# Kernel tuning notes

Hardware: AMD Instinct MI355X
Metric: run time of the kernel (lower is better)

Reference implementation:

```python
import jax, jax.numpy as jnp
import numpy as np

SC = 19          # window stride/size (non-kitti)
K = 3 * SC       # 57, unfold kernel size
CH = 128         # chnn

def conv2d(x, w, b=None, pad=(0, 0)):
    y = jax.lax.conv_general_dilated(
        x, w, (1, 1), [(pad[0], pad[0]), (pad[1], pad[1])],
        dimension_numbers=('NCHW', 'OIHW', 'NCHW'))
    return y if b is None else y + b[None, :, None, None]

def unfold(x):
    # nn.Unfold(kernel_size=3*SC, padding=SC, stride=SC) -> [b, c, K*K, h_sc*w_sc]
    b, c, h, w = x.shape
    h_sc, w_sc = h // SC, w // SC
    xp = jnp.pad(x, ((0, 0), (0, 0), (SC, SC), (SC, SC)))
    ii = np.arange(h_sc)[:, None] * SC + np.arange(K)[None, :]
    jj = np.arange(w_sc)[:, None] * SC + np.arange(K)[None, :]
    p = xp[:, :, ii, :][:, :, :, :, jj]              # [b,c,h_sc,K,w_sc,K]
    return p.transpose(0, 1, 3, 5, 2, 4).reshape(b, c, K * K, h_sc * w_sc)

def to_windows(x):
    # [b,c,h,w] -> [b,c,h_sc*w_sc, SC*SC] (non-overlapping SCxSC windows)
    b, c, h, w = x.shape
    h_sc, w_sc = h // SC, w // SC
    return x.reshape(b, c, h_sc, SC, w_sc, SC).transpose(0, 1, 2, 4, 3, 5).reshape(b, c, h_sc * w_sc, SC * SC)

def fs_kernel(w_prelu, b, h, w):
    # geometric falloff kernel, separable in x/y: [b, K*K, L, SC*SC]
    a = w_prelu[0] * 0.02      # scp = 0.02
    half = 2.0 * SC            # half_ker
    crd = jnp.arange(K, dtype=jnp.float32)
    idx_x = SC + jnp.arange(w, dtype=jnp.float32) % SC
    idx_y = SC + jnp.arange(h, dtype=jnp.float32) % SC
    def falloff(d):
        v = d - half
        pre = jnp.where(v > 0, v, a * v)   # PReLU
        return jnp.maximum(1.0 - pre, 0.0) # -prelu + b(=1), clamped at 0
    ox = falloff(jnp.abs(crd[:, None] - idx_x[None, :]))  # [K, w]
    oy = falloff(jnp.abs(crd[:, None] - idx_y[None, :]))  # [K, h]
    ker = oy[:, None, :, None] * ox[None, :, None, :]      # [Ky, Kx, h, w]
    ker = jnp.broadcast_to(ker[None], (b, K, K, h, w)).reshape(b, K * K, h, w)
    return to_windows(ker)

def kpa(feat_ci, feat_mi, w_qk, w_v, gamma, w_prelu):
    b, c, h_in, w_in = feat_mi.shape
    x_pad = SC - w_in % SC
    y_pad = SC - h_in % SC
    pad4 = ((0, 0), (0, 0), (0, y_pad), (0, x_pad))
    feat_c = jnp.pad(feat_ci, pad4)
    feat_m = jnp.pad(feat_mi, pad4)
    h, w = h_in + y_pad, w_in + x_pad
    h_sc, w_sc = h // SC, w // SC
    # validity mask -> additive -99 bias for padded keys/queries
    fm = jnp.pad(jnp.ones((1, 1, h_in, w_in), feat_mi.dtype), pad4)
    fm_k = unfold(fm)                                  # [1,1,K^2,L]
    fm_q = to_windows(fm)                              # [1,1,L,SC^2]
    am = (fm_k[:, 0, :, :, None] * fm_q[:, 0, None, :, :] - 1.0) * 99.0
    # itr == 0 path: compute attention
    qk = conv2d(feat_c, w_qk)
    feat_q, feat_k = qk[:, :c], qk[:, c:]
    feat_k = unfold(feat_k) * (c ** -0.5)              # [b,c,K^2,L]
    feat_q = to_windows(feat_q)                        # [b,c,L,SC^2]
    attn = jnp.einsum('bckn,bcns->bkns', feat_k, feat_q) + am
    attn = jax.nn.softmax(fs_kernel(w_prelu, b, h, w) * attn, axis=1)
    feat_v = unfold(conv2d(feat_m, w_v))               # [b,c,K^2,L]
    feat_r = jnp.einsum('bkns,bckn->bcns', attn, feat_v)  # [b,c,L,SC^2]
    feat_r = feat_r.reshape(b, c, h_sc, w_sc, SC, SC).transpose(0, 1, 2, 4, 3, 5).reshape(b, c, h, w)
    return feat_mi + feat_r[:, :, :h_in, :w_in] * gamma[0]

def sep_conv_gru(h, x, wz1, bz1, wr1, br1, wq1, bq1, wz2, bz2, wr2, br2, wq2, bq2):
    hx = jnp.concatenate([h, x], 1)
    z = jax.nn.sigmoid(conv2d(hx, wz1, bz1, (0, 2)))
    r = jax.nn.sigmoid(conv2d(hx, wr1, br1, (0, 2)))
    q = jnp.tanh(conv2d(jnp.concatenate([r * h, x], 1), wq1, bq1, (0, 2)))
    h = (1 - z) * h + z * q
    hx = jnp.concatenate([h, x], 1)
    z = jax.nn.sigmoid(conv2d(hx, wz2, bz2, (2, 0)))
    r = jax.nn.sigmoid(conv2d(hx, wr2, br2, (2, 0)))
    q = jnp.tanh(conv2d(jnp.concatenate([r * h, x], 1), wq2, bq2, (2, 0)))
    return (1 - z) * h + z * q

PARAM_SHAPES = [
    ('w_cor1', (256, 324, 1, 1)), ('b_cor1', (256,)), ('w_cor2', (192, 256, 3, 3)), ('b_cor2', (192,)),
    ('w_flo1', (128, 2, 7, 7)), ('b_flo1', (128,)), ('w_flo2', (64, 128, 3, 3)), ('b_flo2', (64,)),
    ('w_mo', (126, 256, 3, 3)), ('b_mo', (126,)),
    ('w_qk', (256, 128, 1, 1)), ('w_v', (128, 128, 1, 1)),
    ('wz1', (128, 512, 1, 5)), ('bz1', (128,)), ('wr1', (128, 512, 1, 5)), ('br1', (128,)),
    ('wq1', (128, 512, 1, 5)), ('bq1', (128,)),
    ('wz2', (128, 512, 5, 1)), ('bz2', (128,)), ('wr2', (128, 512, 5, 1)), ('br2', (128,)),
    ('wq2', (128, 512, 5, 1)), ('bq2', (128,)),
    ('w_f1', (256, 128, 3, 3)), ('b_f1', (256,)), ('w_f2', (2, 256, 3, 3)), ('b_f2', (2,)),
    ('w_m1', (256, 128, 3, 3)), ('b_m1', (256,)), ('w_m2', (576, 256, 1, 1)), ('b_m2', (576,)),
]

def setup_inputs() -> dict:
    key = jax.random.key(0)
    B, H, W = 2, 55, 128
    ks = jax.random.split(key, len(PARAM_SHAPES) + 4)
    inp = {
        'net': jax.random.normal(ks[0], (B, CH, H, W), jnp.float32),
        'inp': jax.random.normal(ks[1], (B, CH, H, W), jnp.float32),
        'corr': jax.random.normal(ks[2], (B, 324, H, W), jnp.float32),
        'flow': jax.random.normal(ks[3], (B, 2, H, W), jnp.float32),
    }
    for i, (name, shp) in enumerate(PARAM_SHAPES):
        fan_in = int(np.prod(shp[1:])) if len(shp) > 1 else shp[0]
        scale = 1.0 / np.sqrt(fan_in) if len(shp) > 1 else 0.01
        inp[name] = scale * jax.random.normal(ks[4 + i], shp, jnp.float32)
    inp['gamma'] = jnp.array([0.5], jnp.float32)            # nonzero so KPA contributes
    inp['w_prelu'] = jnp.array([1.0 / 28.0], jnp.float32)    # 1 / h_k, h_k = (3*SC-1)/2
    inp['itr'] = 0
    return inp

def reference(net, inp, corr, flow, w_cor1, b_cor1, w_cor2, b_cor2, w_flo1, b_flo1, w_flo2, b_flo2, w_mo, b_mo, w_qk, w_v, wz1, bz1, wr1, br1, wq1, bq1, wz2, bz2, wr2, br2, wq2, bq2, w_f1, b_f1, w_f2, b_f2, w_m1, b_m1, w_m2, b_m2, gamma, w_prelu, itr):
    # _mo_enc
    fc = jax.nn.relu(conv2d(corr, w_cor1, b_cor1))
    fc = jax.nn.relu(conv2d(fc, w_cor2, b_cor2, (1, 1)))
    ff = jax.nn.relu(conv2d(flow, w_flo1, b_flo1, (3, 3)))
    ff = jax.nn.relu(conv2d(ff, w_flo2, b_flo2, (1, 1)))
    fm = jax.nn.relu(conv2d(jnp.concatenate([fc, ff], 1), w_mo, b_mo, (1, 1)))
    feat_mo = jnp.concatenate([fm, flow], 1)           # [b,128,h,w]
    # KPA attention (itr == 0)
    feat_moa = kpa(inp, feat_mo, w_qk, w_v, gamma, w_prelu)
    x = jnp.concatenate([inp, feat_mo, feat_moa], 1)   # [b,384,h,w]
    net = sep_conv_gru(net, x, wz1, bz1, wr1, br1, wq1, bq1, wz2, bz2, wr2, br2, wq2, bq2)
    d = jax.nn.relu(conv2d(net, w_f1, b_f1, (1, 1)))
    delta_flow = conv2d(d, w_f2, b_f2, (1, 1))
    m = jax.nn.relu(conv2d(net, w_m1, b_m1, (1, 1)))
    mask = 0.25 * conv2d(m, w_m2, b_m2)
    return net, mask, delta_flow
```

## Files before the change

### kernel.cpp

```cpp
#include <hip/hip_runtime.h>
#include <hip/hip_bf16.h>

typedef __bf16 bf16;
typedef __attribute__((ext_vector_type(8))) __bf16 v8bf;
typedef __attribute__((ext_vector_type(4))) float f32x4;
typedef __attribute__((ext_vector_type(16))) float f32x16;

#define HH 55
#define WW 128
#define HWP 7040
#define BHW 14080
#define QS 0.08838834764831845f
#define LOG2E 1.4426950408889634f

__device__ __forceinline__ void g2l16(const bf16* g, bf16* l){
  __builtin_amdgcn_global_load_lds(
      (const __attribute__((address_space(1))) void*)g,
      (__attribute__((address_space(3))) void*)l, 16, 0, 0);
}

#define NCV 17
__device__ const int PK_CinSrc[NCV] = {324,256,128,256,128,128,512,512,512,512,512,512,128,128,256,256,98};
__device__ const int PK_Kc[NCV]     = {384,256,128,256,128,128,512,512,512,512,512,512,128,128,256,256,128};
__device__ const int PK_ntap[NCV]   = {1,9,9,9,1,1,5,5,5,5,5,5,9,9,9,1,1};
__device__ const int PK_Ctot[NCV]   = {256,256,128,128,256,128,256,256,128,256,256,128,512,512,128,640,128};
__device__ const int PK_coB[NCV]    = {0,0,0,0,0,0,0,128,0,0,128,0,0,256,0,0,0};
__device__ const int PK_dst[NCV]    = {0,98304,688128,835584,1130496,1163264,1179648,1179648,
  1835008,2162688,2162688,2818048,3145728,3145728,3735552,4030464,4194304};
__device__ const int PKD_cum[NCV+1] = {0,98304,540672,614400,904704,937472,953856,
  1281536,1609216,1936896,2264576,2592256,2919936,3214848,3509760,3514368,3661824,3678208};
__device__ const int PKD_Co[NCV]    = {256,192,64,126,256,128,128,128,128,128,128,128,256,256,2,576,128};

__device__ const int PB_off[15]={0,256,512,640,1152,1280,1408,1536,1664,1792,1920,2176,2432,2560,3200};
__device__ const int PB_cnt[15]={256,192,64,126,128,128,128,128,128,128,256,256,2,576,128};

struct W17 { const float* w[17]; };
struct B15 { const float* b[15]; };

struct XP {
  W17 wp; B15 bp;
  const float *net, *inp, *corr, *flow;
  bf16 *Bp; float *bias;
  bf16 *hx; float *hcur; bf16 *corr_cl; bf16 *im2c;
};

__global__ __launch_bounds__(256) void init_k(XP X){
  __shared__ float T[64][65];
  int bid = blockIdx.x;
  const int t = threadIdx.x;
  if (bid < 14368){
    int idx = bid*256 + t;
    int c = 0;
    while (idx >= PKD_cum[c+1]) ++c;
    int local = idx - PKD_cum[c];
    if (c == 16){
      int co = local >> 7, k = local & 127;
      if (k < 98)
        X.Bp[PK_dst[16] + co*128 + k] = (bf16)X.wp.w[16][co*98 + (k&1)*49 + (k>>1)];
      return;
    }
    int Kc = PK_Kc[c];
    int CKc = PKD_Co[c]*Kc;
    int tap = local / CKc;
    int rem = local - tap*CKc;
    int co = rem / Kc;
    int ci = rem - co*Kc;
    int cs = PK_CinSrc[c];
    if (ci < cs){
      float v = X.wp.w[c][(co*cs + ci)*PK_ntap[c] + tap];
      if (c == 4 && co < 128) v *= QS;
      X.Bp[PK_dst[c] + (tap*PK_Ctot[c] + PK_coB[c] + co)*Kc + ci] = (bf16)v;
    }
    return;
  }
  bid -= 14368;
  if (bid < 880){
    int pt = bid%110, ct = (bid/110)&3, b = bid/440;
    const float* src = (ct < 2) ? X.net : X.inp;
    int c0s = (ct & 1)*64;
    int cbase = (ct < 2) ? 0 : 128;
    int p0 = pt*64;
    int pj = t & 63, cr4 = t >> 6;
#pragma unroll
    for (int i=0;i<16;++i)
      T[cr4 + i*4][pj] = src[((size_t)b*128 + c0s + cr4 + i*4)*HWP + p0 + pj];
    __syncthreads();
    int cj = t & 63, pr4 = t >> 6;
#pragma unroll
    for (int i=0;i<16;++i){
      int pp = p0 + pr4 + i*4;
      float v = T[cj][pr4 + i*4];
      X.hx[((size_t)(b*HWP+pp))*512 + cbase + c0s + cj] = (bf16)v;
      if (ct < 2) X.hcur[((size_t)(b*HWP+pp))*128 + c0s + cj] = v;
    }
    return;
  }
  bid -= 880;
  if (bid < 1320){
    int pt = bid%110, ct = (bid/110)%6, b = bid/660;
    int p0 = pt*64, c0s = ct*64;
    int pj = t & 63, cr4 = t >> 6;
#pragma unroll
    for (int i=0;i<16;++i){
      int c = c0s + cr4 + i*4;
      float v = 0.f;
      if (c < 324) v = X.corr[((size_t)b*324 + c)*HWP + p0 + pj];
      T[cr4 + i*4][pj] = v;
    }
    __syncthreads();
    int cj = t & 63, pr4 = t >> 6;
#pragma unroll
    for (int i=0;i<16;++i){
      int pp = p0 + pr4 + i*4;
      int cc = c0s + cj;
      X.corr_cl[((size_t)(b*HWP+pp))*384 + cc] = (bf16)T[cj][pr4 + i*4];
    }
    return;
  }
  bid -= 1320;
  if (bid < 110){
    int i = bid*256 + t;
    int c = i & 1, p = i >> 1;
    int b = p / HWP, pix = p - b*HWP;
    X.hx[(size_t)p*512 + 382 + c] = (bf16)X.flow[(b*2+c)*HWP + pix];
    return;
  }
  bid -= 110;
  if (bid < 7040){
    int i = bid*256 + t;
    int k = i & 127, p = i >> 7;
    int b = p / HWP, pix = p - b*HWP, y = pix >> 7, x = pix & 127;
    float v = 0.f;
    if (k < 98){
      int tap = k >> 1, c2 = k & 1, kh = tap/7, kw = tap - 7*(tap/7);
      int yy = y + kh - 3, xx = x + kw - 3;
      if ((unsigned)yy < 55u && (unsigned)xx < 128u) v = X.flow[(b*2+c2)*HWP + yy*128 + xx];
    }
    X.im2c[i] = (bf16)v;
    return;
  }
  for (int e=0;e<15;++e)
    for (int o=t; o<PB_cnt[e]; o+=256)
      X.bias[PB_off[e]+o] = X.bp.b[e][o];
}

__global__ __launch_bounds__(256) void transp_v(
    const bf16* __restrict__ src, bf16* __restrict__ dst)
{
  int pt = blockIdx.x, ct = blockIdx.y, b = blockIdx.z;
  __shared__ unsigned short T[64][66];
  int t = threadIdx.x;
  int p0 = pt*64, c0s = ct*64;
  int cj = t & 63, pr4 = t >> 6;
#pragma unroll
  for (int i=0;i<16;++i){
    int pp = p0 + pr4 + i*4;
    T[cj][pr4 + i*4] = ((const unsigned short*)src)[((size_t)(b*HWP+pp))*128 + c0s + cj];
  }
  __syncthreads();
  int pj = t & 63, cr4 = t >> 6;
#pragma unroll
  for (int i=0;i<16;++i){
    int cc = c0s + cr4 + i*4;
    ((unsigned short*)dst)[((size_t)(b*128 + cc))*HWP + p0 + pj] = T[cr4 + i*4][pj];
  }
}

struct GP {
  const bf16* A; const bf16* A2;
  const bf16* Bp; const float* bias;
  void* outp; const float* auxZ; float* auxH; float* auxN;
  int Astride, A2stride, Asplit;
  int outCtot, outC0, Nvalid, Kc, CtotPad, tapcode, act, outmode, ntiles, ntOff;
  float scale;
};

__global__ __launch_bounds__(256) void gemm_conv(GP ga, GP gb, const bf16* __restrict__ zp)
{
  const int Mt = blockIdx.x;
  int nt = blockIdx.y;
  const bool useB = (nt >= ga.ntiles);
  if (useB) nt -= ga.ntiles;
  const bf16* A        = useB ? gb.A : ga.A;
  const bf16* A2       = useB ? gb.A2 : ga.A2;
  const bf16* Bp       = useB ? gb.Bp : ga.Bp;
  const float* bias    = useB ? gb.bias : ga.bias;
  void* outp           = useB ? gb.outp : ga.outp;
  const float* auxZ    = useB ? gb.auxZ : ga.auxZ;
  float* auxH          = useB ? gb.auxH : ga.auxH;
  float* auxN          = useB ? gb.auxN : ga.auxN;
  const int Astride    = useB ? gb.Astride : ga.Astride;
  const int A2stride   = useB ? gb.A2stride : ga.A2stride;
  const int Asplit     = useB ? gb.Asplit : ga.Asplit;
  const int outCtot    = useB ? gb.outCtot : ga.outCtot;
  const int outC0      = useB ? gb.outC0 : ga.outC0;
  const int Nvalid     = useB ? gb.Nvalid : ga.Nvalid;
  const int Kc         = useB ? gb.Kc : ga.Kc;
  const int CtotPad    = useB ? gb.CtotPad : ga.CtotPad;
  const int tapcode    = useB ? gb.tapcode : ga.tapcode;
  const int act        = useB ? gb.act : ga.act;
  const int outmode    = useB ? gb.outmode : ga.outmode;
  const int ntOff      = useB ? gb.ntOff : ga.ntOff;
  const float scale    = useB ? gb.scale : ga.scale;

  const int bimg = Mt/110;
  const int rem = Mt - bimg*110;
  const int yy0 = rem >> 1;
  const int xh  = (rem & 1) << 6;
  const int tid = threadIdx.x;
  const int lane = tid & 63, wave = tid >> 6;
  const int wm = wave >> 1, wn = wave & 1;
  const int lr = lane & 15, lq2 = lane >> 4;

  __shared__ __align__(16) bf16 Al[2][4096];
  __shared__ __align__(16) bf16 Bl[2][8192];

  f32x4 acc[2][4];
#pragma unroll
  for (int m=0;m<2;++m)
#pragma unroll
    for (int n=0;n<4;++n) acc[m][n] = (f32x4){0.f,0.f,0.f,0.f};

  const int ntap = (tapcode==0) ? 1 : (tapcode==1 ? 9 : 5);
  const int nsteps = ntap*(Kc>>6);

  const int srow = tid >> 3;
  const int sc   = tid & 7;

#define STAGE(BUF, T, KC) { \
    int ddy, ddx; \
    if (tapcode==0){ ddy=0; ddx=0; } \
    else if (tapcode==1){ ddy=(T)/3-1; ddx=(T)-3*((T)/3)-1; } \
    else if (tapcode==2){ ddy=0; ddx=(T)-2; } \
    else { ddy=(T)-2; ddx=0; } \
    int ysrc = yy0 + ddy; \
    bool yok = (unsigned)ysrc < 55u; \
    const bf16* Abase; int Astr; \
    if ((KC) < Asplit){ Astr = A2stride; \
      Abase = A2 + (size_t)((bimg*55+ysrc)*128)*Astr + (KC); } \
    else { Astr = Astride; \
      Abase = A + (size_t)((bimg*55+ysrc)*128)*Astr + (KC); } \
    _Pragma("unroll") \
    for (int is=0; is<2; ++is){ \
      int r = is*32 + srow; \
      int cc = sc ^ (r&7); \
      int gx = xh + r + ddx; \
      const bf16* srcp = (yok && (unsigned)gx < 128u) ? \
          (Abase + (size_t)gx*Astr + cc*8) : (zp + cc*8); \
      g2l16(srcp, &Al[BUF][is*2048 + wave*512]); \
    } \
    const bf16* Bt = Bp + (size_t)((T)*CtotPad + (nt+ntOff)*128)*Kc + (KC); \
    _Pragma("unroll") \
    for (int is=0; is<4; ++is){ \
      int r = is*32 + srow; \
      int cc = sc ^ (r&7); \
      g2l16(Bt + (size_t)r*Kc + cc*8, &Bl[BUF][is*2048 + wave*512]); \
    } }

  STAGE(0, 0, 0);
  __syncthreads();

  int tcur = 0, kcc = 0;
  for (int si=0; si<nsteps; ++si){
    int kn = kcc + 64, tn = tcur;
    if (kn == Kc){ kn = 0; tn = tcur + 1; }
    if (si + 1 < nsteps){ STAGE((si+1)&1, tn, kn); }
    __builtin_amdgcn_sched_barrier(0);
    kcc = kn; tcur = tn;
    const bf16* Ac = Al[si&1];
    const bf16* Bc = Bl[si&1];
#pragma unroll
    for (int kk=0; kk<2; ++kk){
      v8bf af[2], bfr[4];
#pragma unroll
      for (int m=0;m<2;++m){
        int row = wm*32 + m*16 + lr;
        af[m] = *(const v8bf*)(Ac + row*64 + (((kk*4+lq2) ^ (row&7))<<3));
      }
#pragma unroll
      for (int n=0;n<4;++n){
        int row = wn*64 + n*16 + lr;
        bfr[n] = *(const v8bf*)(Bc + row*64 + (((kk*4+lq2) ^ (row&7))<<3));
      }
#pragma unroll
      for (int m=0;m<2;++m)
#pragma unroll
        for (int n=0;n<4;++n)
          acc[m][n] = __builtin_amdgcn_mfma_f32_16x16x32_bf16(af[m], bfr[n], acc[m][n], 0,0,0);
    }
    __syncthreads();
  }
#undef STAGE

  const size_t pixbase = (size_t)(bimg*55 + yy0)*128 + xh;
#pragma unroll
  for (int nn=0; nn<4; ++nn){
    int cog = (nt+ntOff)*128 + wn*64 + nn*16 + lr;
    float bvl = bias[cog];
    bool cok = cog < Nvalid;
#pragma unroll
    for (int m=0;m<2;++m){
      int rowx = wm*32 + m*16 + lq2*4;
      f32x4 v = acc[m][nn];
#pragma unroll
      for (int r=0;r<4;++r){
        float vv = v[r] + bvl;
        if (act==1)      vv = fmaxf(vv, 0.f);
        else if (act==2) vv = 1.f/(1.f+__expf(-vv));
        else if (act==3) vv = tanhf(vv);
        vv *= scale;
        if (cok){
          int prow = rowx + r;
          size_t p = pixbase + prow;
          if (outmode==0)      ((bf16*)outp)[p*outCtot + outC0 + cog] = (bf16)vv;
          else if (outmode==1) ((float*)outp)[p*outCtot + outC0 + cog] = vv;
          else if (outmode==2) ((float*)outp)[((size_t)bimg*outCtot + outC0 + cog)*HWP + yy0*128 + xh + prow] = vv;
          else if (outmode==3){
            int c = cog & 127;
            ((bf16*)outp)[p*128 + c] = (bf16)(vv * auxH[p*128 + c]);
          } else {
            int c = cog;
            float z  = auxZ[p*128 + c];
            float h0 = auxH[p*128 + c];
            float hn = (1.f - z)*h0 + z*vv;
            auxH[p*128 + c] = hn;
            ((bf16*)outp)[p*512 + c] = (bf16)hn;
            if (auxN){
              int pixloc = (int)(p - (size_t)bimg*HWP);
              auxN[((size_t)bimg*128 + c)*HWP + pixloc] = hn;
            }
          }
        }
      }
    }
  }
}

__global__ __launch_bounds__(256) void gemm_n16(
    const bf16* __restrict__ A, int Astride,
    const bf16* __restrict__ Bp, const float* __restrict__ bias,
    float* __restrict__ outp, int outCtot, int Kc, int CtotPad)
{
  const int Mt = blockIdx.x;
  const int bimg = Mt/110;
  const int rem = Mt - bimg*110;
  const int yy0 = rem >> 1;
  const int xh  = (rem & 1) << 6;
  const int tid = threadIdx.x;
  const int wave = tid >> 6, lane = tid & 63;
  const int lr = lane & 15, lq2 = lane >> 4;

  __shared__ __align__(16) bf16 Al[4][2560];
  __shared__ __align__(16) bf16 Bl[4][640];
  __shared__ float Rd[4][1024];

  bf16* Alw = Al[wave];
  bf16* Blw = Bl[wave];

  f32x4 acc[4];
#pragma unroll
  for (int m=0;m<4;++m) acc[m] = (f32x4){0.f,0.f,0.f,0.f};

  const int brw = lane >> 2, bc = lane & 3;
  uint4 av[4]; uint4 bv;

#define PFN(SI) { \
    int T_ = (SI) >> 3, KC = ((SI)&7)*32; \
    int ddy = T_/3 - 1, ddx = T_ - 3*(T_/3) - 1; \
    int ysrc = yy0 + ddy; int gx = xh + lane + ddx; \
    bool ok = (unsigned)ysrc < 55u && (unsigned)gx < 128u; \
    const bf16* Ap = A + (size_t)((bimg*55+ysrc)*128 + gx)*Astride + KC; \
    av[0] = ok ? *(const uint4*)(Ap)      : make_uint4(0,0,0,0); \
    av[1] = ok ? *(const uint4*)(Ap + 8)  : make_uint4(0,0,0,0); \
    av[2] = ok ? *(const uint4*)(Ap + 16) : make_uint4(0,0,0,0); \
    av[3] = ok ? *(const uint4*)(Ap + 24) : make_uint4(0,0,0,0); \
    bv = *(const uint4*)(Bp + (size_t)(T_*CtotPad + brw)*Kc + KC + bc*8); }

  const int s0 = wave*18;
  PFN(s0);
  for (int si=s0; si<s0+18; ++si){
    *(uint4*)(Alw + lane*40 + 0)  = av[0];
    *(uint4*)(Alw + lane*40 + 8)  = av[1];
    *(uint4*)(Alw + lane*40 + 16) = av[2];
    *(uint4*)(Alw + lane*40 + 24) = av[3];
    *(uint4*)(Blw + brw*40 + bc*8) = bv;
    if (si + 1 < s0+18) PFN(si+1);
    v8bf bq = *(const v8bf*)(Blw + lr*40 + lq2*8);
#pragma unroll
    for (int m=0;m<4;++m){
      v8bf af = *(const v8bf*)(Alw + (m*16 + lr)*40 + lq2*8);
      acc[m] = __builtin_amdgcn_mfma_f32_16x16x32_bf16(af, bq, acc[m], 0,0,0);
    }
  }
#undef PFN

#pragma unroll
  for (int m=0;m<4;++m)
    *(f32x4*)&Rd[wave][lane*16 + m*4] = acc[m];
  __syncthreads();
  if (wave == 0 && lr < 2){
    float bvl = bias[lr];
#pragma unroll
    for (int m=0;m<4;++m)
#pragma unroll
      for (int r=0;r<4;++r){
        int ix = lane*16 + m*4 + r;
        float s = Rd[0][ix] + Rd[1][ix] + Rd[2][ix] + Rd[3][ix];
        int row = m*16 + lq2*4 + r;
        outp[((size_t)bimg*outCtot + lr)*HWP + yy0*128 + xh + row] = s + bvl;
      }
  }
}

__global__ __launch_bounds__(256,1) void attn_k(
    const bf16* __restrict__ QK, const bf16* __restrict__ Vt,
    bf16* __restrict__ hx,
    const float* __restrict__ gammap, const float* __restrict__ wprelup)
{
  __shared__ __align__(16) float SM[16640];
  const int tid = threadIdx.x;
  const int wv = tid >> 6, lane = tid & 63;
  const int lq = lane & 31, hi = lane >> 5;
  const int blk = blockIdx.x;
  const int qt = blk % 12;
  const int n  = (blk/12) % 21;
  const int b  = blk / 252;
  const int hs = n/7, wd = n - 7*hs;
  const int y0 = (hs-1)*19, x0 = (wd-1)*19;
  const int rylo = max(0, y0), ryhi = min(54, y0+56);
  const int rxlo = max(0, x0), rxhi = min(127, x0+56);
  const int rxA  = rxlo & ~7;
  const int s = qt*32 + lq;
  const int sy = s/19, sx = s - sy*19;
  const int qy = y0 + 19 + sy, qx = x0 + 19 + sx;
  const int qpix = (b*55 + min(qy,54))*128 + min(qx,127);
  const float a = wprelup[0]*0.02f;
  const float qyf = (float)qy;

  bf16* Kl = (bf16*)SM + wv*8192;
  bf16* Vl = Kl + 4096;

  v8bf qf[8];
#pragma unroll
  for (int ks=0; ks<8; ++ks)
    qf[ks] = *(const v8bf*)(QK + (size_t)qpix*256 + ks*16 + hi*8);

  float fx0[16], fx1[16];
  unsigned msk0 = 0, msk1 = 0;
  {
    float dxq0 = (float)(rxA - qx);
    int xl0 = rxlo - rxA, xm0 = rxhi - rxA;
#pragma unroll
    for (int r=0;r<16;++r){
      int Ri = (r&3) + 8*(r>>2) + 4*hi;
      float dxv = fabsf(dxq0 + (float)Ri) - 38.f;
      fx0[r] = fmaxf(1.f - fmaxf(dxv, a*dxv), 0.f);
      if (Ri >= xl0 && Ri <= xm0) msk0 |= 1u<<r;
      float dxv1 = fabsf(dxq0 + 32.f + (float)Ri) - 38.f;
      fx1[r] = fmaxf(1.f - fmaxf(dxv1, a*dxv1), 0.f);
      int Ri1 = Ri + 32;
      if (Ri1 >= xl0 && Ri1 <= xm0) msk1 |= 1u<<r;
    }
  }

  f32x16 acc[4];
#pragma unroll
  for (int nf=0; nf<4; ++nf)
#pragma unroll
    for (int r=0;r<16;++r) acc[nf][r] = 0.f;
  float m2 = -40.f, den = 0.f;

  const int nry = (ryhi - rylo - wv)/4 + 1;
  const int nit = nry*2;

#define ISSUE_K(RY, RX) { int pixK = (b*55+(RY))*128 + (RX); \
  _Pragma("unroll") \
  for (int i=0;i<8;++i){ \
    int key = i*4 + (lane>>4); int cs = (lane&15) ^ (key&7); \
    g2l16(QK + (size_t)(pixK+key)*256 + 128 + cs*8, Kl + i*512); } }
#define ISSUE_V(RY, RX) { \
  _Pragma("unroll") \
  for (int i=0;i<8;++i){ \
    int ch = i*16 + (lane>>2); int cs = (lane&3) ^ ((ch>>1)&3); \
    g2l16(Vt + (size_t)(b*128+ch)*HWP + (RY)*128 + (RX) + cs*8, Vl + i*512); } }

  ISSUE_K(rylo + wv, rxA);

  for (int it=0; it<nit; ++it){
    const int ry  = rylo + wv + (it>>1)*4;
    const int tpar = it & 1;
    asm volatile("s_waitcnt lgkmcnt(0)" ::: "memory");
    __builtin_amdgcn_sched_barrier(0);
    asm volatile("s_waitcnt vmcnt(0)" ::: "memory");
    __builtin_amdgcn_sched_barrier(0);
    ISSUE_V(ry, rxA + tpar*32);
    __builtin_amdgcn_sched_barrier(0);

    f32x16 Cs, Cs2;
#pragma unroll
    for (int r=0;r<16;++r){ Cs[r] = 0.f; Cs2[r] = 0.f; }
    __builtin_amdgcn_s_setprio(1);
#pragma unroll
    for (int ks=0; ks<4; ++ks){
      v8bf kf = *(const v8bf*)(Kl + lq*128 + (((ks*2+hi) ^ (lq&7))<<3));
      Cs = __builtin_amdgcn_mfma_f32_32x32x16_bf16(kf, qf[ks], Cs, 0,0,0);
    }
#pragma unroll
    for (int ks=4; ks<8; ++ks){
      v8bf kf = *(const v8bf*)(Kl + lq*128 + (((ks*2+hi) ^ (lq&7))<<3));
      Cs2 = __builtin_amdgcn_mfma_f32_32x32x16_bf16(kf, qf[ks], Cs2, 0,0,0);
    }
    __builtin_amdgcn_s_setprio(0);
    float pr[16];
    {
      float dyv = fabsf((float)ry - qyf) - 38.f;
      float fy = fmaxf(1.f - fmaxf(dyv, a*dyv), 0.f);
      float fyk = fy * LOG2E;
      unsigned mk = tpar ? msk1 : msk0;
      float l2v[16]; float tmax = -1e30f;
#pragma unroll
      for (int r=0;r<16;++r){
        float fx = tpar ? fx1[r] : fx0[r];
        float lv = fyk * fx * (Cs[r] + Cs2[r]);
        lv = ((mk>>r)&1u) ? lv : -1e30f;
        l2v[r] = lv;
        tmax = fmaxf(tmax, lv);
      }
      tmax = fmaxf(tmax, __shfl_xor(tmax, 32));
      if (__any(tmax > m2 + 11.f)){
        float m2n = fmaxf(m2, tmax);
        float sc = exp2f(m2 - m2n);
        den *= sc;
#pragma unroll
        for (int r=0;r<16;++r){
          float scr = __shfl(sc, (r&3) + 8*(r>>2) + 4*hi);
          acc[0][r]*=scr; acc[1][r]*=scr; acc[2][r]*=scr; acc[3][r]*=scr;
        }
        m2 = m2n;
      }
#pragma unroll
      for (int r=0;r<16;++r){
        pr[r] = exp2f(l2v[r] - m2);
        den += pr[r];
      }
    }
    asm volatile("s_waitcnt lgkmcnt(0)" ::: "memory");
    __builtin_amdgcn_sched_barrier(0);
    asm volatile("s_waitcnt vmcnt(0)" ::: "memory");
    __builtin_amdgcn_sched_barrier(0);
    if (it + 1 < nit){
      int ryn = rylo + wv + ((it+1)>>1)*4;
      ISSUE_K(ryn, rxA + ((it+1)&1)*32);
      __builtin_amdgcn_sched_barrier(0);
    }
    float po[8], po2[8];
#pragma unroll
    for (int r=0;r<8;++r) po[r]  = __shfl_xor(pr[r],   32);
#pragma unroll
    for (int r=0;r<8;++r) po2[r] = __shfl_xor(pr[r+8], 32);
    v8bf pa0, pa1;
#pragma unroll
    for (int j=0;j<4;++j){
      pa0[j]   = (bf16)(hi ? po[j+4]  : pr[j]);
      pa0[j+4] = (bf16)(hi ? pr[j+4]  : po[j]);
      pa1[j]   = (bf16)(hi ? po2[j+4] : pr[j+8]);
      pa1[j+4] = (bf16)(hi ? pr[j+12] : po2[j]);
    }
    __builtin_amdgcn_s_setprio(1);
#pragma unroll
    for (int nf=0; nf<4; ++nf){
      int ch = nf*32 + lq;
      int sw = (lq>>1)&3;
      v8bf v0 = *(const v8bf*)(Vl + ch*32 + ((hi     ^ sw)<<3));
      v8bf v1 = *(const v8bf*)(Vl + ch*32 + (((2+hi) ^ sw)<<3));
      acc[nf] = __builtin_amdgcn_mfma_f32_32x32x16_bf16(pa0, v0, acc[nf], 0,0,0);
      acc[nf] = __builtin_amdgcn_mfma_f32_32x32x16_bf16(pa1, v1, acc[nf], 0,0,0);
    }
    __builtin_amdgcn_s_setprio(0);
  }
#undef ISSUE_K
#undef ISSUE_V
  den += __shfl_xor(den, 32);

  float* Osh = SM;
  float* Msh = SM + 16384;
  float* Dsh = SM + 16512;
  __syncthreads();
#pragma unroll
  for (int nf=0; nf<4; ++nf)
#pragma unroll
    for (int r=0;r<16;++r)
      Osh[(wv*32 + (r&3) + 8*(r>>2) + 4*hi)*128 + nf*32 + lq] = acc[nf][r];
  if (hi == 0){ Msh[wv*32 + lq] = m2; Dsh[wv*32 + lq] = den; }
  __syncthreads();

  int q = tid >> 3, co = (tid & 7)*16;
  float m0 = Msh[q], m1 = Msh[32+q], mm2 = Msh[64+q], m3 = Msh[96+q];
  float M = fmaxf(fmaxf(m0,m1), fmaxf(mm2,m3));
  float s0 = exp2f(m0-M), s1 = exp2f(m1-M), s2 = exp2f(mm2-M), s3 = exp2f(m3-M);
  int ss = qt*32 + q;
  float dent = s0*Dsh[q] + s1*Dsh[32+q] + s2*Dsh[64+q] + s3*Dsh[96+q];
  int sy2 = ss/19, sx2 = ss - sy2*19;
  int qy2 = y0 + 19 + sy2, qx2 = x0 + 19 + sx2;
  if (ss < 361 && qy2 < 55 && qx2 < 128){
    size_t pix = (size_t)(b*55+qy2)*128 + qx2;
    float g = gammap[0] / dent;
#pragma unroll
    for (int c=0;c<16;++c){
      float o = s0*Osh[q*128+co+c] + s1*Osh[(32+q)*128+co+c]
              + s2*Osh[(64+q)*128+co+c] + s3*Osh[(96+q)*128+co+c];
      float fm = (float)hx[pix*512 + 256 + co + c];
      hx[pix*512 + 384 + co + c] = (bf16)(fm + o*g);
    }
  }
}

static inline GP mkgp(const bf16* A, int Astride, const bf16* Bp, const float* bias,
                      void* outp, int outCtot, int outC0, int Nvalid, int Kc, int CtotPad,
                      int tapcode, int act, int outmode, float scale, int ntiles){
  GP g{};
  g.A=A; g.A2=A; g.Astride=Astride; g.A2stride=Astride; g.Asplit=0;
  g.Bp=Bp; g.bias=bias; g.outp=outp; g.auxZ=nullptr; g.auxH=nullptr; g.auxN=nullptr;
  g.outCtot=outCtot; g.outC0=outC0; g.Nvalid=Nvalid; g.Kc=Kc; g.CtotPad=CtotPad;
  g.tapcode=tapcode; g.act=act; g.outmode=outmode; g.ntiles=ntiles; g.ntOff=0;
  g.scale=scale;
  return g;
}

extern "C" void kernel_launch(void* const* d_in, const int* in_sizes, int n_in,
                              void* d_out, int out_size, void* d_ws, size_t ws_size,
                              hipStream_t stream) {
  const float* net   = (const float*)d_in[0];
  const float* inp   = (const float*)d_in[1];
  const float* corr  = (const float*)d_in[2];
  const float* flow  = (const float*)d_in[3];
  const float* w_cor1=(const float*)d_in[4];  const float* b_cor1=(const float*)d_in[5];
  const float* w_cor2=(const float*)d_in[6];  const float* b_cor2=(const float*)d_in[7];
  const float* w_flo1=(const float*)d_in[8];  const float* b_flo1=(const float*)d_in[9];
  const float* w_flo2=(const float*)d_in[10]; const float* b_flo2=(const float*)d_in[11];
  const float* w_mo  =(const float*)d_in[12]; const float* b_mo  =(const float*)d_in[13];
  const float* w_qk  =(const float*)d_in[14];
  const float* w_v   =(const float*)d_in[15];
  const float* wz1=(const float*)d_in[16]; const float* bz1=(const float*)d_in[17];
  const float* wr1=(const float*)d_in[18]; const float* br1=(const float*)d_in[19];
  const float* wq1=(const float*)d_in[20]; const float* bq1=(const float*)d_in[21];
  const float* wz2=(const float*)d_in[22]; const float* bz2=(const float*)d_in[23];
  const float* wr2=(const float*)d_in[24]; const float* br2=(const float*)d_in[25];
  const float* wq2=(const float*)d_in[26]; const float* bq2=(const float*)d_in[27];
  const float* w_f1=(const float*)d_in[28]; const float* b_f1=(const float*)d_in[29];
  const float* w_f2=(const float*)d_in[30]; const float* b_f2=(const float*)d_in[31];
  const float* w_m1=(const float*)d_in[32]; const float* b_m1=(const float*)d_in[33];
  const float* w_m2=(const float*)d_in[34]; const float* b_m2=(const float*)d_in[35];
  const float* gamma  =(const float*)d_in[36];
  const float* w_prelu=(const float*)d_in[37];

  float* ws = (float*)d_ws;
  bf16* hx     = (bf16*)ws;
  bf16* BPp    = (bf16*)(ws + 3604480);
  float* BIASp = ws + 5709824;
  const bf16* zp = (const bf16*)(ws + 5713152);
  const size_t S0 = 5713216;
  bf16* corr_cl = (bf16*)(ws + S0);
  bf16* fc1o    = (bf16*)(ws + S0 + 2703360);
  bf16* catB    = (bf16*)(ws + S0 + 4505600);
  bf16* ff1o    = (bf16*)(ws + S0 + 6307840);
  bf16* im2c    = (bf16*)(ws + S0 + 7208960);
  float* hcur   = ws + S0 + 8110080;
  bf16* QKb    = (bf16*)(ws + S0);
  bf16* Vb     = (bf16*)(ws + S0 + 1810432);
  bf16* Vt     = (bf16*)(ws + S0 + 2711552);
  float* zb    = ws + S0;
  bf16* rhb    = (bf16*)(ws + S0 + 3604480);
  bf16* dm     = (bf16*)(ws + S0);

  float* out_net  = (float*)d_out;
  float* out_mask = out_net + 1802240;
  float* out_df   = out_net + 9912320;

  dim3 blk(256);

  hipMemsetAsync(ws + 3604480, 0, (size_t)8434944, stream);
  XP X{};
  const float* wl[17] = {w_cor1,w_cor2,w_flo2,w_mo,w_qk,w_v,wz1,wr1,wq1,wz2,wr2,wq2,w_f1,w_m1,w_f2,w_m2,w_flo1};
  const float* bl[15] = {b_cor1,b_cor2,b_flo2,b_mo,bz1,br1,bq1,bz2,br2,bq2,b_f1,b_m1,b_f2,b_m2,b_flo1};
  for (int i=0;i<17;++i) X.wp.w[i]=wl[i];
  for (int i=0;i<15;++i) X.bp.b[i]=bl[i];
  X.net=net; X.inp=inp; X.corr=corr; X.flow=flow;
  X.Bp=BPp; X.bias=BIASp; X.hx=hx; X.hcur=hcur; X.corr_cl=corr_cl; X.im2c=im2c;
  init_k<<<dim3(14368+880+1320+110+7040+1),blk,0,stream>>>(X);

  GP g0{};

  {
    GP a = mkgp(corr_cl,384, BPp+0,       BIASp+0,    fc1o,256,0,256, 384,256, 0,1,0,1.f, 2);
    GP b = mkgp(im2c,128,    BPp+4194304, BIASp+3200, ff1o,128,0,128, 128,128, 0,1,0,1.f, 1);
    gemm_conv<<<dim3(220,3),blk,0,stream>>>(a, b, zp);
  }
  {
    GP a = mkgp(fc1o,256,    BPp+98304,   BIASp+256,  catB,256,0,192, 256,256, 1,1,0,1.f, 2);
    GP b = mkgp(ff1o,128,    BPp+688128,  BIASp+512,  catB,256,192,64,128,128, 1,1,0,1.f, 1);
    gemm_conv<<<dim3(220,3),blk,0,stream>>>(a, b, zp);
  }
  {
    GP a = mkgp(catB,256,    BPp+835584,  BIASp+640,  hx,  512,256,126,256,128, 1,1,0,1.f, 1);
    gemm_conv<<<dim3(220,1),blk,0,stream>>>(a, g0, zp);
  }

  {
    GP a = mkgp(hx+128,512,  BPp+1130496, BIASp+768,  QKb, 256,0,256, 128,256, 0,0,0,1.f, 2);
    GP b = mkgp(hx+256,512,  BPp+1163264, BIASp+1024, Vb,  128,0,128, 128,128, 0,0,0,1.f, 1);
    gemm_conv<<<dim3(220,3),blk,0,stream>>>(a, b, zp);
  }
  transp_v<<<dim3(110,2,2),blk,0,stream>>>(Vb, Vt);
  attn_k<<<dim3(504),blk,0,stream>>>(QKb, Vt, hx, gamma, w_prelu);

  {
    GP a = mkgp(hx,512,      BPp+1179648, BIASp+1152, zb,  128,0,128, 512,256, 2,2,1,1.f, 1);
    GP b = mkgp(hx,512,      BPp+1179648, BIASp+1152, rhb, 0,0,256,   512,256, 2,2,3,1.f, 1);
    b.ntOff = 1; b.auxH = hcur;
    gemm_conv<<<dim3(220,2),blk,0,stream>>>(a, b, zp);
  }
  {
    GP a = mkgp(hx,512,      BPp+1835008, BIASp+1408, hx,  0,0,128,   512,128, 2,3,4,1.f, 1);
    a.A2 = rhb; a.A2stride = 128; a.Asplit = 128;
    a.auxZ = zb; a.auxH = hcur; a.auxN = nullptr;
    gemm_conv<<<dim3(220,1),blk,0,stream>>>(a, g0, zp);
  }

  {
    GP a = mkgp(hx,512,      BPp+2162688, BIASp+1536, zb,  128,0,128, 512,256, 3,2,1,1.f, 1);
    GP b = mkgp(hx,512,      BPp+2162688, BIASp+1536, rhb, 0,0,256,   512,256, 3,2,3,1.f, 1);
    b.ntOff = 1; b.auxH = hcur;
    gemm_conv<<<dim3(220,2),blk,0,stream>>>(a, b, zp);
  }
  {
    GP a = mkgp(hx,512,      BPp+2818048, BIASp+1792, hx,  0,0,128,   512,128, 3,3,4,1.f, 1);
    a.A2 = rhb; a.A2stride = 128; a.Asplit = 128;
    a.auxZ = zb; a.auxH = hcur; a.auxN = out_net;
    gemm_conv<<<dim3(220,1),blk,0,stream>>>(a, g0, zp);
  }

  {
    GP a = mkgp(hx,512,      BPp+3145728, BIASp+1920, dm,  512,0,512, 128,512, 1,1,0,1.f, 4);
    gemm_conv<<<dim3(220,4),blk,0,stream>>>(a, g0, zp);
  }
  gemm_n16 <<<dim3(220),blk,0,stream>>>(dm,512,   BPp+3735552, BIASp+2432, out_df, 2, 256,128);
  {
    GP a = mkgp(dm+256,512,  BPp+4030464, BIASp+2560, out_mask,576,0,576,256,640, 0,0,2,0.25f, 5);
    gemm_conv<<<dim3(220,5),blk,0,stream>>>(a, g0, zp);
  }
}
```

Before: 552.2 us.

## Stage GEMM epilogue through LDS for coalesced stores; remap attention blocks; simplify QK chain

The GEMM epilogue for outmodes 0 and 2 now writes results into shared memory (swizzled for bf16) and then stores them with 16-byte vector writes, replacing scattered per-element global stores. The attention kernel remaps block indices so that consecutive blocks are spread across different windows and images. It also merges the two split QK MFMA accumulators into a single chain and removes the s_setprio hints. The single chain adds a serial dependency across eight MFMAs, and the epilogue adds an extra barrier and LDS round trip.

```diff
diff --git a/kernel.cpp b/kernel.cpp
--- a/kernel.cpp
+++ b/kernel.cpp
@@ -293,41 +293,116 @@
 #undef STAGE
 
   const size_t pixbase = (size_t)(bimg*55 + yy0)*128 + xh;
-#pragma unroll
-  for (int nn=0; nn<4; ++nn){
-    int cog = (nt+ntOff)*128 + wn*64 + nn*16 + lr;
-    float bvl = bias[cog];
-    bool cok = cog < Nvalid;
-#pragma unroll
-    for (int m=0;m<2;++m){
-      int rowx = wm*32 + m*16 + lq2*4;
-      f32x4 v = acc[m][nn];
-#pragma unroll
-      for (int r=0;r<4;++r){
-        float vv = v[r] + bvl;
-        if (act==1)      vv = fmaxf(vv, 0.f);
-        else if (act==2) vv = 1.f/(1.f+__expf(-vv));
-        else if (act==3) vv = tanhf(vv);
-        vv *= scale;
-        if (cok){
-          int prow = rowx + r;
-          size_t p = pixbase + prow;
-          if (outmode==0)      ((bf16*)outp)[p*outCtot + outC0 + cog] = (bf16)vv;
-          else if (outmode==1) ((float*)outp)[p*outCtot + outC0 + cog] = vv;
-          else if (outmode==2) ((float*)outp)[((size_t)bimg*outCtot + outC0 + cog)*HWP + yy0*128 + xh + prow] = vv;
-          else if (outmode==3){
-            int c = cog & 127;
-            ((bf16*)outp)[p*128 + c] = (bf16)(vv * auxH[p*128 + c]);
-          } else {
-            int c = cog;
-            float z  = auxZ[p*128 + c];
-            float h0 = auxH[p*128 + c];
-            float hn = (1.f - z)*h0 + z*vv;
-            auxH[p*128 + c] = hn;
-            ((bf16*)outp)[p*512 + c] = (bf16)hn;
-            if (auxN){
-              int pixloc = (int)(p - (size_t)bimg*HWP);
-              auxN[((size_t)bimg*128 + c)*HWP + pixloc] = hn;
+  if (outmode == 0){
+    bf16* Ost = (bf16*)Al;
+#pragma unroll
+    for (int nn=0; nn<4; ++nn){
+      int colL = wn*64 + nn*16 + lr;
+      float bvl = bias[(nt+ntOff)*128 + colL];
+#pragma unroll
+      for (int m=0;m<2;++m){
+        int rowx = wm*32 + m*16 + lq2*4;
+        f32x4 v = acc[m][nn];
+#pragma unroll
+        for (int r=0;r<4;++r){
+          float vv = v[r] + bvl;
+          if (act==1)      vv = fmaxf(vv, 0.f);
+          else if (act==2) vv = 1.f/(1.f+__expf(-vv));
+          else if (act==3) vv = tanhf(vv);
+          vv *= scale;
+          int row = rowx + r;
+          int pch = (colL>>3) ^ (row & 7);
+          Ost[row*128 + (pch<<3) + (colL&7)] = (bf16)vv;
+        }
+      }
+    }
+    __syncthreads();
+    {
+      int rowl = tid >> 2, seg = tid & 3;
+      size_t p = pixbase + rowl;
+      bf16* dstp = (bf16*)outp + p*outCtot + outC0 + (nt+ntOff)*128 + seg*32;
+      const bf16* srcr = Ost + rowl*128;
+      int cb = (nt+ntOff)*128 + seg*32;
+#pragma unroll
+      for (int k2=0;k2<4;++k2){
+        int pch = (seg*4 + k2) ^ (rowl & 7);
+        int cog = cb + k2*8;
+        if (cog + 8 <= Nvalid)
+          *(uint4*)(dstp + k2*8) = *(const uint4*)(srcr + (pch<<3));
+        else if (cog < Nvalid){
+          const bf16* s8 = srcr + (pch<<3);
+          for (int e=0; e<Nvalid-cog; ++e) dstp[k2*8+e] = s8[e];
+        }
+      }
+    }
+  } else if (outmode == 2){
+    float* Ost2 = (float*)Bl;
+#pragma unroll
+    for (int nn=0; nn<4; ++nn){
+      int chL = wn*64 + nn*16 + lr;
+      float bvl = bias[(nt+ntOff)*128 + chL];
+#pragma unroll
+      for (int m=0;m<2;++m){
+        int rowx = wm*32 + m*16 + lq2*4;
+        f32x4 v = acc[m][nn];
+#pragma unroll
+        for (int r=0;r<4;++r){
+          float vv = v[r] + bvl;
+          if (act==1)      vv = fmaxf(vv, 0.f);
+          else if (act==2) vv = 1.f/(1.f+__expf(-vv));
+          else if (act==3) vv = tanhf(vv);
+          Ost2[chL*64 + rowx + r] = vv*scale;
+        }
+      }
+    }
+    __syncthreads();
+    {
+      int ch = tid >> 1, half = tid & 1;
+      int cog = (nt+ntOff)*128 + ch;
+      if (cog < Nvalid){
+        float* dstp = (float*)outp + ((size_t)bimg*outCtot + outC0 + cog)*HWP
+                    + yy0*128 + xh + half*32;
+        const float* srcr = Ost2 + ch*64 + half*32;
+#pragma unroll
+        for (int k2=0;k2<8;++k2)
+          *(uint4*)(dstp + k2*4) = *(const uint4*)(srcr + k2*4);
+      }
+    }
+  } else {
+#pragma unroll
+    for (int nn=0; nn<4; ++nn){
+      int cog = (nt+ntOff)*128 + wn*64 + nn*16 + lr;
+      float bvl = bias[cog];
+      bool cok = cog < Nvalid;
+#pragma unroll
+      for (int m=0;m<2;++m){
+        int rowx = wm*32 + m*16 + lq2*4;
+        f32x4 v = acc[m][nn];
+#pragma unroll
+        for (int r=0;r<4;++r){
+          float vv = v[r] + bvl;
+          if (act==1)      vv = fmaxf(vv, 0.f);
+          else if (act==2) vv = 1.f/(1.f+__expf(-vv));
+          else if (act==3) vv = tanhf(vv);
+          vv *= scale;
+          if (cok){
+            int prow = rowx + r;
+            size_t p = pixbase + prow;
+            if (outmode==1) ((float*)outp)[p*outCtot + outC0 + cog] = vv;
+            else if (outmode==3){
+              int c = cog & 127;
+              ((bf16*)outp)[p*128 + c] = (bf16)(vv * auxH[p*128 + c]);
+            } else {
+              int c = cog;
+              float z  = auxZ[p*128 + c];
+              float h0 = auxH[p*128 + c];
+              float hn = (1.f - z)*h0 + z*vv;
+              auxH[p*128 + c] = hn;
+              ((bf16*)outp)[p*512 + c] = (bf16)hn;
+              if (auxN){
+                int pixloc = (int)(p - (size_t)bimg*HWP);
+                auxN[((size_t)bimg*128 + c)*HWP + pixloc] = hn;
+              }
             }
           }
         }
@@ -421,7 +496,8 @@
   const int tid = threadIdx.x;
   const int wv = tid >> 6, lane = tid & 63;
   const int lq = lane & 31, hi = lane >> 5;
-  const int blk = blockIdx.x;
+  const int blk0 = blockIdx.x;
+  const int blk = (blk0 & 7)*63 + (blk0 >> 3);
   const int qt = blk % 12;
   const int n  = (blk/12) % 21;
   const int b  = blk / 252;
@@ -496,21 +572,14 @@
     ISSUE_V(ry, rxA + tpar*32);
     __builtin_amdgcn_sched_barrier(0);
 
-    f32x16 Cs, Cs2;
-#pragma unroll
-    for (int r=0;r<16;++r){ Cs[r] = 0.f; Cs2[r] = 0.f; }
-    __builtin_amdgcn_s_setprio(1);
-#pragma unroll
-    for (int ks=0; ks<4; ++ks){
+    f32x16 Cs;
+#pragma unroll
+    for (int r=0;r<16;++r) Cs[r] = 0.f;
+#pragma unroll
+    for (int ks=0; ks<8; ++ks){
       v8bf kf = *(const v8bf*)(Kl + lq*128 + (((ks*2+hi) ^ (lq&7))<<3));
       Cs = __builtin_amdgcn_mfma_f32_32x32x16_bf16(kf, qf[ks], Cs, 0,0,0);
     }
-#pragma unroll
-    for (int ks=4; ks<8; ++ks){
-      v8bf kf = *(const v8bf*)(Kl + lq*128 + (((ks*2+hi) ^ (lq&7))<<3));
-      Cs2 = __builtin_amdgcn_mfma_f32_32x32x16_bf16(kf, qf[ks], Cs2, 0,0,0);
-    }
-    __builtin_amdgcn_s_setprio(0);
     float pr[16];
     {
       float dyv = fabsf((float)ry - qyf) - 38.f;
@@ -521,7 +590,7 @@
 #pragma unroll
       for (int r=0;r<16;++r){
         float fx = tpar ? fx1[r] : fx0[r];
-        float lv = fyk * fx * (Cs[r] + Cs2[r]);
+        float lv = fyk * fx * Cs[r];
         lv = ((mk>>r)&1u) ? lv : -1e30f;
         l2v[r] = lv;
         tmax = fmaxf(tmax, lv);
@@ -566,7 +635,6 @@
       pa1[j]   = (bf16)(hi ? po2[j+4] : pr[j+8]);
       pa1[j+4] = (bf16)(hi ? pr[j+12] : po2[j]);
     }
-    __builtin_amdgcn_s_setprio(1);
 #pragma unroll
     for (int nf=0; nf<4; ++nf){
       int ch = nf*32 + lq;
@@ -576,7 +644,6 @@
       acc[nf] = __builtin_amdgcn_mfma_f32_32x32x16_bf16(pa0, v0, acc[nf], 0,0,0);
       acc[nf] = __builtin_amdgcn_mfma_f32_32x32x16_bf16(pa1, v1, acc[nf], 0,0,0);
     }
-    __builtin_amdgcn_s_setprio(0);
   }
 #undef ISSUE_K
 #undef ISSUE_V
```

After: 544.9 us. Within noise of the previous version (-1.3%).
